# Optimization experiments

Measured on AMD Instinct MI355X. Metric: run time of the kernel, lower is better.

Reference implementation:

```python
import jax, jax.numpy as jnp
import numpy as np

U, V, A = 100000, 50000, 5000   # n_users, n_videos, n_vloggers
D = 64                           # latent_dim_rec
N_LAYERS = 3                     # VAGNN_n_layers
NNZ_UI, NNZ_UA, NNZ_G2, NNZ_G4 = 4_000_000, 2_000_000, 200_000, 2_000_000
BATCH = 1024

def spmm(rows, cols, vals, x, n_rows):
    # sparse.mm(COO(rows, cols, vals), x) -> [n_rows, d]
    return jax.ops.segment_sum(vals[:, None] * x[cols], rows, num_segments=n_rows)

def one_propagate(rows, cols, vals, a_feat, b_feat):
    # LightGCN propagation: mean over layer-0..n embeddings (running sum, no stack)
    n = a_feat.shape[0] + b_feat.shape[0]
    feats = jnp.concatenate([a_feat, b_feat], axis=0)
    acc, cur = feats, feats
    for _ in range(N_LAYERS):
        cur = spmm(rows, cols, vals, cur, n)
        acc = acc + cur
    light = acc / (N_LAYERS + 1)
    return light[:a_feat.shape[0]], light[a_feat.shape[0]:]

def l2norm(x):
    # F.normalize(x, dim=1), eps=1e-12
    return x / jnp.maximum(jnp.linalg.norm(x, axis=1, keepdims=True), 1e-12)

def setup_inputs() -> dict:
    key = jax.random.key(0)
    ks = jax.random.split(key, 16)
    return {
        'emb_user':    jax.random.normal(ks[0], (U, D), jnp.float32) * 0.1,
        'emb_video':   jax.random.normal(ks[1], (V, D), jnp.float32) * 0.1,
        'emb_vlogger': jax.random.normal(ks[2], (A, D), jnp.float32) * 0.1,
        'q':           jax.random.normal(ks[3], (D, D), jnp.float32) * 0.1,
        'ui_rows': jax.random.randint(ks[4], (NNZ_UI,), 0, U + V, jnp.int32),
        'ui_cols': jax.random.randint(ks[5], (NNZ_UI,), 0, U + V, jnp.int32),
        'ui_vals': jax.random.uniform(ks[6], (NNZ_UI,), jnp.float32) * 0.01,
        'ua_rows': jax.random.randint(ks[7], (NNZ_UA,), 0, U + A, jnp.int32),
        'ua_cols': jax.random.randint(ks[8], (NNZ_UA,), 0, U + A, jnp.int32),
        'ua_vals': jax.random.uniform(ks[9], (NNZ_UA,), jnp.float32) * 0.01,
        'g2_rows': jax.random.randint(ks[10], (NNZ_G2,), 0, A, jnp.int32),
        'g2_cols': jax.random.randint(ks[11], (NNZ_G2,), 0, V, jnp.int32),
        'g2_vals': jax.random.uniform(ks[12], (NNZ_G2,), jnp.float32) * 0.01,
        'g4_rows': jax.random.randint(ks[13], (NNZ_G4,), 0, V, jnp.int32),
        'g4_cols': jax.random.randint(ks[14], (NNZ_G4,), 0, U, jnp.int32),
        'g4_vals': jax.random.uniform(ks[15], (NNZ_G4,), jnp.float32) * 0.01,
        'vlogger_list': jax.random.randint(jax.random.fold_in(key, 100), (V,), 0, A, jnp.int32),
        'users': jax.random.randint(jax.random.fold_in(key, 101), (BATCH,), 0, U, jnp.int32),
    }

def reference(emb_user, emb_video, emb_vlogger, q,
              ui_rows, ui_cols, ui_vals,
              ua_rows, ua_cols, ua_vals,
              g2_rows, g2_cols, g2_vals,
              g4_rows, g4_cols, g4_vals,
              vlogger_list, users):
    # computer()
    atom_u, atom_v = one_propagate(ui_rows, ui_cols, ui_vals, emb_user, emb_video)
    atom_a = l2norm(spmm(g2_rows, g2_cols, g2_vals, atom_v, A))
    non_u, non_a = one_propagate(ua_rows, ua_cols, ua_vals, emb_user, emb_vlogger)
    non_v = l2norm(spmm(g4_rows, g4_cols, g4_vals, non_u, V))
    # getUsersRating()
    u_a, u_n = atom_u[users], non_u[users]                 # [B, D]
    vl_a, vl_n = atom_a[vlogger_list], non_a[vlogger_list]  # [V, D]
    ui = jax.nn.sigmoid(u_a @ atom_v.T + u_n @ non_v.T)      # [B, V]
    ua = jax.nn.sigmoid(u_a @ vl_a.T + u_n @ vl_n.T)         # [B, V]
    vid = (atom_v + non_v) * 0.5
    vlog = (vl_a + vl_n) * 0.5
    w = jax.nn.sigmoid(jnp.sum((vid @ q) * vlog, axis=1))    # [V]
    return w * ui + (1.0 - w) * ua
```

## Files before the change

### kernel.cpp

```cpp
#include <hip/hip_runtime.h>
#include <hip/hip_bf16.h>

#define U_N 100000
#define V_N 50000
#define A_N 5000

typedef float4 f4;
typedef unsigned int u32;
typedef __attribute__((ext_vector_type(8))) short bf16x8;
typedef __attribute__((ext_vector_type(4))) float f32x4;

__device__ inline float bflo(u32 p) { return __uint_as_float(p << 16); }
__device__ inline float bfhi(u32 p) { return __uint_as_float(p & 0xffff0000u); }
__device__ inline u32 f2bf(float f) {
  u32 u = __float_as_uint(f);
  return (u + 0x7fffu + ((u >> 16) & 1u)) >> 16;
}
__device__ inline u32 pack2(float lo, float hi) {
  return f2bf(lo) | (f2bf(hi) << 16);
}
__device__ inline bf16x8 ld8(const u32* p) {
  uint4 u = *(const uint4*)p;
  return __builtin_bit_cast(bf16x8, u);
}

__global__ void k_concat2b(const float* __restrict__ a, int na,
                           const float* __restrict__ b, int nb,
                           u32* __restrict__ curH, float* __restrict__ acc) {
  int total4 = (na + nb) * 16;
  for (int i = blockIdx.x * blockDim.x + threadIdx.x; i < total4;
       i += gridDim.x * blockDim.x) {
    int fi = i * 4;
    f4 v = (fi < na * 64) ? *(const f4*)(a + fi)
                          : *(const f4*)(b + (fi - na * 64));
    *(f4*)(acc + fi) = v;
    uint2 h; h.x = pack2(v.x, v.y); h.y = pack2(v.z, v.w);
    *(uint2*)(curH + (fi >> 1)) = h;
  }
}

__global__ void k_count(const int* __restrict__ rows, int nnz, int* __restrict__ cnt) {
  for (int i = blockIdx.x * blockDim.x + threadIdx.x; i < nnz;
       i += gridDim.x * blockDim.x)
    atomicAdd(&cnt[rows[i]], 1);
}

__global__ void k_bsum(const int* __restrict__ cnt, int n, int* __restrict__ bsum) {
  __shared__ int red[1024];
  int t = threadIdx.x;
  int i = blockIdx.x * 1024 + t;
  red[t] = (i < n) ? cnt[i] : 0;
  __syncthreads();
  for (int off = 512; off; off >>= 1) {
    if (t < off) red[t] += red[t + off];
    __syncthreads();
  }
  if (t == 0) bsum[blockIdx.x] = red[0];
}

__global__ void k_bscan(int* __restrict__ bsum, int nb) {
  if (threadIdx.x == 0) {
    int run = 0;
    for (int i = 0; i < nb; ++i) {
      int c = bsum[i];
      bsum[i] = run;
      run += c;
    }
  }
}

__global__ void k_bapply(const int* __restrict__ cnt, int n,
                         const int* __restrict__ bsum,
                         int* __restrict__ rp, int* __restrict__ pos) {
  __shared__ int sc[1024];
  int t = threadIdx.x;
  int i = blockIdx.x * 1024 + t;
  int c = (i < n) ? cnt[i] : 0;
  sc[t] = c;
  __syncthreads();
  #pragma unroll
  for (int off = 1; off < 1024; off <<= 1) {
    int v = (t >= off) ? sc[t - off] : 0;
    __syncthreads();
    sc[t] += v;
    __syncthreads();
  }
  int val = bsum[blockIdx.x] + sc[t] - c;
  if (i < n) {
    rp[i] = val;
    pos[i] = val;
    if (i == n - 1) rp[n] = val + c;
  }
}

__global__ void k_fillw(const int* __restrict__ rows, const int* __restrict__ cols,
                        const float* __restrict__ vals, int nnz,
                        int* __restrict__ pos, int2* __restrict__ ep,
                        int nrows, int win) {
  int tid = blockIdx.x * blockDim.x + threadIdx.x;
  int stride = gridDim.x * blockDim.x;
  for (int r0 = 0; r0 < nrows; r0 += win) {
    int r1 = min(r0 + win, nrows);
    for (int i = tid; i < nnz; i += stride) {
      int r = rows[i];
      if (r >= r0 && r < r1) {
        int slot = atomicAdd(&pos[r], 1);
        ep[slot] = make_int2(cols[i], __float_as_int(vals[i]));
      }
    }
  }
}

__global__ void k_mark(const int* __restrict__ users, int nb,
                       int* __restrict__ flag, int* __restrict__ rcount,
                       int* __restrict__ rlist) {
  int b = blockIdx.x * blockDim.x + threadIdx.x;
  if (b < nb) {
    int u = users[b];
    if (atomicExch(&flag[u], 1) == 0) {
      int m = atomicAdd(rcount, 1);
      rlist[m] = u;
    }
  }
}

__device__ __forceinline__ void spmm_row(
    int row, const int* __restrict__ rp, const int2* __restrict__ ep,
    const u32* __restrict__ inH, int instrU,
    u32* __restrict__ outH, int ostrU, int ocolU,
    float* __restrict__ acc, int l2n, int wout, int lane, int eg, int du) {
  int e0 = rp[row], e1 = rp[row + 1];
  float s[8] = {0.f, 0.f, 0.f, 0.f, 0.f, 0.f, 0.f, 0.f};
  int e = e0 + eg;
  for (; e + 8 < e1; e += 16) {
    int2 ed0 = ep[e];
    int2 ed1 = ep[e + 8];
    float v0 = __int_as_float(ed0.y), v1 = __int_as_float(ed1.y);
    uint4 x0 = *(const uint4*)(inH + (size_t)ed0.x * instrU + du);
    uint4 x1 = *(const uint4*)(inH + (size_t)ed1.x * instrU + du);
    s[0] = fmaf(v0, bflo(x0.x), s[0]); s[1] = fmaf(v0, bfhi(x0.x), s[1]);
    s[2] = fmaf(v0, bflo(x0.y), s[2]); s[3] = fmaf(v0, bfhi(x0.y), s[3]);
    s[4] = fmaf(v0, bflo(x0.z), s[4]); s[5] = fmaf(v0, bfhi(x0.z), s[5]);
    s[6] = fmaf(v0, bflo(x0.w), s[6]); s[7] = fmaf(v0, bfhi(x0.w), s[7]);
    s[0] = fmaf(v1, bflo(x1.x), s[0]); s[1] = fmaf(v1, bfhi(x1.x), s[1]);
    s[2] = fmaf(v1, bflo(x1.y), s[2]); s[3] = fmaf(v1, bfhi(x1.y), s[3]);
    s[4] = fmaf(v1, bflo(x1.z), s[4]); s[5] = fmaf(v1, bfhi(x1.z), s[5]);
    s[6] = fmaf(v1, bflo(x1.w), s[6]); s[7] = fmaf(v1, bfhi(x1.w), s[7]);
  }
  if (e < e1) {
    int2 ed0 = ep[e];
    float v0 = __int_as_float(ed0.y);
    uint4 x0 = *(const uint4*)(inH + (size_t)ed0.x * instrU + du);
    s[0] = fmaf(v0, bflo(x0.x), s[0]); s[1] = fmaf(v0, bfhi(x0.x), s[1]);
    s[2] = fmaf(v0, bflo(x0.y), s[2]); s[3] = fmaf(v0, bfhi(x0.y), s[3]);
    s[4] = fmaf(v0, bflo(x0.z), s[4]); s[5] = fmaf(v0, bfhi(x0.z), s[5]);
    s[6] = fmaf(v0, bflo(x0.w), s[6]); s[7] = fmaf(v0, bfhi(x0.w), s[7]);
  }
  #pragma unroll
  for (int j = 0; j < 8; ++j) {
    s[j] += __shfl_xor(s[j], 8);
    s[j] += __shfl_xor(s[j], 16);
    s[j] += __shfl_xor(s[j], 32);
  }
  if (l2n) {
    float ss = 0.f;
    #pragma unroll
    for (int j = 0; j < 8; ++j) ss = fmaf(s[j], s[j], ss);
    ss += __shfl_xor(ss, 1);
    ss += __shfl_xor(ss, 2);
    ss += __shfl_xor(ss, 4);
    float inv = 1.0f / fmaxf(sqrtf(ss), 1e-12f);
    #pragma unroll
    for (int j = 0; j < 8; ++j) s[j] *= inv;
  }
  if (eg == 0) {
    if (wout) {
      uint4 o;
      o.x = pack2(s[0], s[1]); o.y = pack2(s[2], s[3]);
      o.z = pack2(s[4], s[5]); o.w = pack2(s[6], s[7]);
      *(uint4*)(outH + (size_t)row * ostrU + ocolU + du) = o;
    }
    if (acc) {
      float* ap = acc + (size_t)row * 64 + (lane & 7) * 8;
      f4 a0 = *(f4*)ap, a1 = *(f4*)(ap + 4);
      a0.x += s[0]; a0.y += s[1]; a0.z += s[2]; a0.w += s[3];
      a1.x += s[4]; a1.y += s[5]; a1.z += s[6]; a1.w += s[7];
      *(f4*)ap = a0; *(f4*)(ap + 4) = a1;
    }
  }
}

__global__ void k_spmm_b(const int* __restrict__ rp, const int2* __restrict__ ep,
                         int nrows, int rbase,
                         const u32* __restrict__ inH, int instrU,
                         u32* __restrict__ outH, int ostrU, int ocolU,
                         float* __restrict__ acc, int l2n, int wout) {
  int lane = threadIdx.x & 63;
  int w = (blockIdx.x * blockDim.x + threadIdx.x) >> 6;
  int nw = (gridDim.x * blockDim.x) >> 6;
  int eg = lane >> 3;
  int du = (lane & 7) * 4;
  for (int r = w; r < nrows; r += nw)
    spmm_row(rbase + r, rp, ep, inH, instrU, outH, ostrU, ocolU, acc, l2n, wout,
             lane, eg, du);
}

__global__ void k_spmm_b_list(const int* __restrict__ rp, const int2* __restrict__ ep,
                              const int* __restrict__ rlist, const int* __restrict__ rcount,
                              const u32* __restrict__ inH, int instrU,
                              float* __restrict__ acc) {
  int lane = threadIdx.x & 63;
  int w = (blockIdx.x * blockDim.x + threadIdx.x) >> 6;
  int nw = (gridDim.x * blockDim.x) >> 6;
  int eg = lane >> 3;
  int du = (lane & 7) * 4;
  int m = *rcount;
  for (int r = w; r < m; r += nw)
    spmm_row(rlist[r], rp, ep, inH, instrU, nullptr, 0, 0, acc, 0, 0,
             lane, eg, du);
}

__global__ void k_scale_ua(float* __restrict__ acc, u32* __restrict__ UAuH) {
  int total4 = (U_N + A_N) * 16;
  for (int i = blockIdx.x * blockDim.x + threadIdx.x; i < total4;
       i += gridDim.x * blockDim.x) {
    int fi = i * 4;
    f4 v = *(f4*)(acc + fi);
    v.x *= 0.25f; v.y *= 0.25f; v.z *= 0.25f; v.w *= 0.25f;
    *(f4*)(acc + fi) = v;
    if (fi < U_N * 64) {
      uint2 h; h.x = pack2(v.x, v.y); h.y = pack2(v.z, v.w);
      *(uint2*)(UAuH + (fi >> 1)) = h;
    }
  }
}

__global__ void k_scale_ui(float* __restrict__ acc, u32* __restrict__ VAH) {
  int total4 = (U_N + V_N) * 16;
  for (int i = blockIdx.x * blockDim.x + threadIdx.x; i < total4;
       i += gridDim.x * blockDim.x) {
    int fi = i * 4;
    f4 v = *(f4*)(acc + fi);
    v.x *= 0.25f; v.y *= 0.25f; v.z *= 0.25f; v.w *= 0.25f;
    *(f4*)(acc + fi) = v;
    if (fi >= U_N * 64) {
      int rem = fi - U_N * 64;
      int row = rem >> 6, col = rem & 63;
      uint2 h; h.x = pack2(v.x, v.y); h.y = pack2(v.z, v.w);
      *(uint2*)(VAH + (size_t)row * 64 + (col >> 1)) = h;
    }
  }
}

__global__ void k_gather_u(const int* __restrict__ users,
                           const float* __restrict__ accUI,
                           const float* __restrict__ accUA,
                           u32* __restrict__ UcatH) {
  int b = blockIdx.x;
  int t = threadIdx.x;
  int u = users[b];
  UcatH[b * 64 + t] = pack2(accUI[(size_t)u * 64 + 2 * t], accUI[(size_t)u * 64 + 2 * t + 1]);
  UcatH[b * 64 + 32 + t] = pack2(accUA[(size_t)u * 64 + 2 * t], accUA[(size_t)u * 64 + 2 * t + 1]);
}

__global__ void k_gather_vb(const int* __restrict__ vlist,
                            const u32* __restrict__ atomAH,
                            const float* __restrict__ accUA,
                            u32* __restrict__ VBH) {
  int v = blockIdx.x * 4 + (threadIdx.x >> 5);
  int t = threadIdx.x & 31;
  int a = vlist[v];
  VBH[(size_t)v * 64 + t] = atomAH[(size_t)a * 32 + t];
  VBH[(size_t)v * 64 + 32 + t] =
      pack2(accUA[(size_t)(U_N + a) * 64 + 2 * t], accUA[(size_t)(U_N + a) * 64 + 2 * t + 1]);
}

__global__ void k_w(const u32* __restrict__ VAH, const u32* __restrict__ VBH,
                    const float* __restrict__ q, float* __restrict__ wv) {
  __shared__ float qs[64 * 64];
  for (int i = threadIdx.x; i < 4096; i += blockDim.x) qs[i] = q[i];
  __syncthreads();
  int lane = threadIdx.x & 63;
  int v = blockIdx.x * 4 + (threadIdx.x >> 6);
  if (v >= V_N) return;
  int half = lane & 1;
  u32 pa0 = VAH[(size_t)v * 64 + (lane >> 1)];
  u32 pa1 = VAH[(size_t)v * 64 + 32 + (lane >> 1)];
  u32 pb0 = VBH[(size_t)v * 64 + (lane >> 1)];
  u32 pb1 = VBH[(size_t)v * 64 + 32 + (lane >> 1)];
  float vid = 0.5f * ((half ? bfhi(pa0) : bflo(pa0)) + (half ? bfhi(pa1) : bflo(pa1)));
  float vlog = 0.5f * ((half ? bfhi(pb0) : bflo(pb0)) + (half ? bfhi(pb1) : bflo(pb1)));
  float s = 0.0f;
  for (int d = 0; d < 64; ++d)
    s = fmaf(__shfl(vid, d, 64), qs[d * 64 + lane], s);
  float t = s * vlog;
  #pragma unroll
  for (int off = 32; off; off >>= 1) t += __shfl_xor(t, off, 64);
  if (lane == 0) wv[v] = 1.0f / (1.0f + __expf(-t));
}

#define SPAD 68
__global__ __launch_bounds__(256) void k_rating_mfma(
    const u32* __restrict__ UcatH, const u32* __restrict__ VAH,
    const u32* __restrict__ VBH, const float* __restrict__ wv,
    float* __restrict__ out) {
  __shared__ u32 sVA[64 * SPAD];
  __shared__ u32 sVB[64 * SPAD];
  int t = threadIdx.x;
  int n0 = blockIdx.x * 64;
  for (int i = t; i < 1024; i += 256) {
    int row = i >> 4, c4 = (i & 15) * 4;
    int v = n0 + row;
    uint4 a = make_uint4(0, 0, 0, 0), b = make_uint4(0, 0, 0, 0);
    if (v < V_N) {
      a = *(const uint4*)(VAH + (size_t)v * 64 + c4);
      b = *(const uint4*)(VBH + (size_t)v * 64 + c4);
    }
    *(uint4*)(&sVA[row * SPAD + c4]) = a;
    *(uint4*)(&sVB[row * SPAD + c4]) = b;
  }
  __syncthreads();
  int lane = t & 63, wave = t >> 6;
  int m0 = (blockIdx.y * 4 + wave) * 32;
  int rr = lane & 15, g = lane >> 4;
  f32x4 accA[2][4], accB[2][4];
  #pragma unroll
  for (int i = 0; i < 2; ++i)
    #pragma unroll
    for (int j = 0; j < 4; ++j) {
      accA[i][j] = (f32x4){0.f, 0.f, 0.f, 0.f};
      accB[i][j] = (f32x4){0.f, 0.f, 0.f, 0.f};
    }
  const u32* uc0 = UcatH + (size_t)(m0 + rr) * 64 + g * 4;
  #pragma unroll
  for (int ks = 0; ks < 4; ++ks) {
    bf16x8 a0 = ld8(uc0 + ks * 16);
    bf16x8 a1 = ld8(uc0 + 16 * 64 + ks * 16);
    #pragma unroll
    for (int j = 0; j < 4; ++j) {
      int so = (j * 16 + rr) * SPAD + ks * 16 + g * 4;
      bf16x8 bA = __builtin_bit_cast(bf16x8, *(const uint4*)(&sVA[so]));
      bf16x8 bB = __builtin_bit_cast(bf16x8, *(const uint4*)(&sVB[so]));
      accA[0][j] = __builtin_amdgcn_mfma_f32_16x16x32_bf16(a0, bA, accA[0][j], 0, 0, 0);
      accA[1][j] = __builtin_amdgcn_mfma_f32_16x16x32_bf16(a1, bA, accA[1][j], 0, 0, 0);
      accB[0][j] = __builtin_amdgcn_mfma_f32_16x16x32_bf16(a0, bB, accB[0][j], 0, 0, 0);
      accB[1][j] = __builtin_amdgcn_mfma_f32_16x16x32_bf16(a1, bB, accB[1][j], 0, 0, 0);
    }
  }
  #pragma unroll
  for (int j = 0; j < 4; ++j) {
    int v = n0 + j * 16 + rr;
    if (v >= V_N) continue;
    float wvv = wv[v];
    #pragma unroll
    for (int i = 0; i < 2; ++i) {
      #pragma unroll
      for (int reg = 0; reg < 4; ++reg) {
        int u = m0 + i * 16 + g * 4 + reg;
        float sa = 1.0f / (1.0f + __expf(-accA[i][j][reg]));
        float sb = 1.0f / (1.0f + __expf(-accB[i][j][reg]));
        __builtin_nontemporal_store(wvv * sa + (1.0f - wvv) * sb,
                                    &out[(size_t)u * V_N + v]);
      }
    }
  }
}

extern "C" void kernel_launch(void* const* d_in, const int* in_sizes, int n_in,
                              void* d_out, int out_size, void* d_ws, size_t ws_size,
                              hipStream_t stream) {
  const float* emb_user    = (const float*)d_in[0];
  const float* emb_video   = (const float*)d_in[1];
  const float* emb_vlogger = (const float*)d_in[2];
  const float* q           = (const float*)d_in[3];
  const int*   ui_rows = (const int*)d_in[4];
  const int*   ui_cols = (const int*)d_in[5];
  const float* ui_vals = (const float*)d_in[6];
  const int*   ua_rows = (const int*)d_in[7];
  const int*   ua_cols = (const int*)d_in[8];
  const float* ua_vals = (const float*)d_in[9];
  const int*   g2_rows = (const int*)d_in[10];
  const int*   g2_cols = (const int*)d_in[11];
  const float* g2_vals = (const float*)d_in[12];
  const int*   g4_rows = (const int*)d_in[13];
  const int*   g4_cols = (const int*)d_in[14];
  const float* g4_vals = (const float*)d_in[15];
  const int*   vlist   = (const int*)d_in[16];
  const int*   users   = (const int*)d_in[17];
  int nnz_ui = in_sizes[4], nnz_ua = in_sizes[7];
  int nnz_g2 = in_sizes[10], nnz_g4 = in_sizes[13];

  float* ws = (float*)d_ws;
  float* accUI = ws;
  float* accUA = ws + 9600000;
  u32*   curH  = (u32*)(ws + 16320000);
  u32*   nxtH  = (u32*)(ws + 21120000);
  u32*   VAH   = (u32*)(ws + 25920000);
  u32*   VBH   = (u32*)(ws + 29120000);
  u32*   UAuH  = (u32*)(ws + 32320000);
  u32*   UcatH = (u32*)(ws + 35520000);
  u32*   atomAH= (u32*)(ws + 35585536);
  float* wv    = ws + 35745536;
  int*   bsum  = (int*)(ws + 35795536);
  int*   ib    = (int*)(ws + 35800000);
  int*   flag   = (int*)VBH;
  int*   rcount = flag + 100000;
  int*   rlist  = flag + 100016;

  const int nUI = U_N + V_N, nUA = U_N + A_N;
  auto nr_pad = [](int nrows) { return (size_t)((nrows + 1 + 15) & ~15); };

  auto build_csr = [&](const int* rows, const int* cols, const float* vals,
                       int nnz, int nrows, int win, int* rp, int* pos, int2* ep) {
    hipMemsetAsync(pos, 0, (size_t)nrows * 4, stream);
    k_count<<<2048, 256, 0, stream>>>(rows, nnz, pos);
    int nb = (nrows + 1023) / 1024;
    k_bsum<<<nb, 1024, 0, stream>>>(pos, nrows, bsum);
    k_bscan<<<1, 64, 0, stream>>>(bsum, nb);
    k_bapply<<<nb, 1024, 0, stream>>>(pos, nrows, bsum, rp, pos);
    k_fillw<<<2048, 256, 0, stream>>>(rows, cols, vals, nnz, pos, ep, nrows, win);
  };

  {
    size_t NR = nr_pad(nUI);
    int* rp = ib; int* pos = ib + NR; int2* ep = (int2*)(ib + 2 * NR);
    build_csr(ui_rows, ui_cols, ui_vals, nnz_ui, nUI, 65536, rp, pos, ep);
    k_concat2b<<<2048, 256, 0, stream>>>(emb_user, U_N, emb_video, V_N, curH, accUI);
    hipMemsetAsync(flag, 0, (size_t)(100016) * 4, stream);
    k_mark<<<4, 256, 0, stream>>>(users, 1024, flag, rcount, rlist);
    k_spmm_b<<<2048, 256, 0, stream>>>(rp, ep, nUI, 0, curH, 32, nxtH, 32, 0, accUI, 0, 1);
    k_spmm_b<<<2048, 256, 0, stream>>>(rp, ep, nUI, 0, nxtH, 32, curH, 32, 0, accUI, 0, 1);
    k_spmm_b<<<2048, 256, 0, stream>>>(rp, ep, V_N, U_N, curH, 32, nullptr, 0, 0, accUI, 0, 0);
    k_spmm_b_list<<<256, 256, 0, stream>>>(rp, ep, rlist, rcount, curH, 32, accUI);
  }
  {
    size_t NR = nr_pad(nUA);
    int* rp = ib; int* pos = ib + NR; int2* ep = (int2*)(ib + 2 * NR);
    build_csr(ua_rows, ua_cols, ua_vals, nnz_ua, nUA, 65536, rp, pos, ep);
    k_concat2b<<<2048, 256, 0, stream>>>(emb_user, U_N, emb_vlogger, A_N, curH, accUA);
    k_spmm_b<<<2048, 256, 0, stream>>>(rp, ep, nUA, 0, curH, 32, nxtH, 32, 0, accUA, 0, 1);
    k_spmm_b<<<2048, 256, 0, stream>>>(rp, ep, nUA, 0, nxtH, 32, curH, 32, 0, accUA, 0, 1);
    k_spmm_b<<<2048, 256, 0, stream>>>(rp, ep, nUA, 0, curH, 32, nullptr, 0, 0, accUA, 0, 0);
  }
  k_scale_ua<<<2048, 256, 0, stream>>>(accUA, UAuH);
  k_scale_ui<<<2048, 256, 0, stream>>>(accUI, VAH);
  size_t NR4 = nr_pad(V_N), NR2 = nr_pad(A_N);
  int* rp4 = ib; int* pos4 = ib + NR4; int2* ep4 = (int2*)(ib + 2 * NR4);
  int* ib2 = (int*)(ep4 + nnz_g4);
  int* rp2 = ib2; int* pos2 = ib2 + NR2; int2* ep2 = (int2*)(ib2 + 2 * NR2);
  build_csr(g4_rows, g4_cols, g4_vals, nnz_g4, V_N, 65536, rp4, pos4, ep4);
  build_csr(g2_rows, g2_cols, g2_vals, nnz_g2, A_N, 65536, rp2, pos2, ep2);
  k_spmm_b<<<2048, 256, 0, stream>>>(rp2, ep2, A_N, 0, VAH, 64, atomAH, 32, 0, nullptr, 1, 1);
  k_spmm_b<<<2048, 256, 0, stream>>>(rp4, ep4, V_N, 0, UAuH, 32, VAH, 64, 32, nullptr, 1, 1);
  k_gather_u<<<1024, 32, 0, stream>>>(users, accUI, accUA, UcatH);
  k_gather_vb<<<12500, 128, 0, stream>>>(vlist, atomAH, accUA, VBH);
  k_w<<<12500, 256, 0, stream>>>(VAH, VBH, q, wv);
  dim3 gridR((V_N + 63) / 64, 1024 / 128);
  k_rating_mfma<<<gridR, 256, 0, stream>>>(UcatH, VAH, VBH, wv, (float*)d_out);
}
```

Before: 1.501 ms.

## Build CSR via binned partition pass then per-bin scatter flush

Replaces the windowed fill kernel, which re-read all COO entries once per 65536-row window, with a two-phase build. A wave-level ballot partition first stages the edges into row-range bins in scratch buffers (reusing the accumulator and embedding buffers). A flush pass then scatters each bin into the CSR, so the atomics and writes stay localized. The small g2 graph uses a simple single-pass fill. This adds an extra staging write and read plus a serial loop over bins per wave, and depends on the reused scratch buffers being dead at that point.

```diff
diff --git a/kernel.cpp b/kernel.cpp
--- a/kernel.cpp
+++ b/kernel.cpp
@@ -93,20 +93,98 @@
   }
 }
 
-__global__ void k_fillw(const int* __restrict__ rows, const int* __restrict__ cols,
-                        const float* __restrict__ vals, int nnz,
-                        int* __restrict__ pos, int2* __restrict__ ep,
-                        int nrows, int win) {
+__global__ void k_fill(const int* __restrict__ rows, const int* __restrict__ cols,
+                       const float* __restrict__ vals, int nnz,
+                       int* __restrict__ pos, int2* __restrict__ ep) {
+  for (int i = blockIdx.x * blockDim.x + threadIdx.x; i < nnz;
+       i += gridDim.x * blockDim.x) {
+    int slot = atomicAdd(&pos[rows[i]], 1);
+    ep[slot] = make_int2(cols[i], __float_as_int(vals[i]));
+  }
+}
+
+__global__ void k_seedb(const int* __restrict__ rp, int binsh, int nbins,
+                        int* __restrict__ bcur) {
+  int b = threadIdx.x;
+  if (b < nbins) bcur[b] = rp[b << binsh];
+}
+
+__global__ void k_part(const int* __restrict__ rows, const int* __restrict__ cols,
+                       const float* __restrict__ vals, int nnz,
+                       int binsh, int nbins, int* __restrict__ bcur,
+                       int4* __restrict__ stg) {
+  int lane = threadIdx.x & 63;
+  int wid = (blockIdx.x * blockDim.x + threadIdx.x) >> 6;
+  int nw = (gridDim.x * blockDim.x) >> 6;
+  int nbatch = (nnz + 1023) >> 10;
+  unsigned long long lmask = (lane == 63) ? 0x7fffffffffffffffull
+                                          : ((1ull << lane) - 1ull);
+  for (int q = wid; q < nbatch; q += nw) {
+    int base = q << 10;
+    int rA[16], cA[16], bA[16];
+    float vA[16];
+    bool full = (base + 1024 <= nnz);
+    #pragma unroll
+    for (int j = 0; j < 4; ++j) {
+      int idx = base + j * 256 + lane * 4;
+      if (full) {
+        int4 r4 = *(const int4*)(rows + idx);
+        int4 c4 = *(const int4*)(cols + idx);
+        f4  v4 = *(const f4*)(vals + idx);
+        rA[j*4+0]=r4.x; rA[j*4+1]=r4.y; rA[j*4+2]=r4.z; rA[j*4+3]=r4.w;
+        cA[j*4+0]=c4.x; cA[j*4+1]=c4.y; cA[j*4+2]=c4.z; cA[j*4+3]=c4.w;
+        vA[j*4+0]=v4.x; vA[j*4+1]=v4.y; vA[j*4+2]=v4.z; vA[j*4+3]=v4.w;
+      } else {
+        #pragma unroll
+        for (int k = 0; k < 4; ++k) {
+          int e = idx + k;
+          if (e < nnz) { rA[j*4+k]=rows[e]; cA[j*4+k]=cols[e]; vA[j*4+k]=vals[e]; }
+          else { rA[j*4+k] = -1; cA[j*4+k] = 0; vA[j*4+k] = 0.f; }
+        }
+      }
+    }
+    #pragma unroll
+    for (int jj = 0; jj < 16; ++jj)
+      bA[jj] = (rA[jj] >= 0) ? (rA[jj] >> binsh) : -1;
+    for (int b = 0; b < nbins; ++b) {
+      unsigned long long m[16];
+      int n[16], tot = 0;
+      #pragma unroll
+      for (int jj = 0; jj < 16; ++jj) {
+        m[jj] = __ballot(bA[jj] == b);
+        n[jj] = __popcll(m[jj]);
+        tot += n[jj];
+      }
+      if (tot == 0) continue;
+      int g = 0;
+      if (lane == 0) g = atomicAdd(&bcur[b], tot);
+      g = __shfl(g, 0, 64);
+      int run = 0;
+      #pragma unroll
+      for (int jj = 0; jj < 16; ++jj) {
+        if (bA[jj] == b) {
+          int off = g + run + __popcll(m[jj] & lmask);
+          stg[off] = make_int4(rA[jj], cA[jj], __float_as_int(vA[jj]), 0);
+        }
+        run += n[jj];
+      }
+    }
+  }
+}
+
+__global__ void k_flush(const int4* __restrict__ stg, const int* __restrict__ rp,
+                        int nrows, int binsh, int nbins,
+                        int* __restrict__ pos, int2* __restrict__ ep) {
   int tid = blockIdx.x * blockDim.x + threadIdx.x;
   int stride = gridDim.x * blockDim.x;
-  for (int r0 = 0; r0 < nrows; r0 += win) {
-    int r1 = min(r0 + win, nrows);
-    for (int i = tid; i < nnz; i += stride) {
-      int r = rows[i];
-      if (r >= r0 && r < r1) {
-        int slot = atomicAdd(&pos[r], 1);
-        ep[slot] = make_int2(cols[i], __float_as_int(vals[i]));
-      }
+  for (int b = 0; b < nbins; ++b) {
+    int s = rp[b << binsh];
+    int r1 = min((b + 1) << binsh, nrows);
+    int e = rp[r1];
+    for (int idx = s + tid; idx < e; idx += stride) {
+      int4 ed = stg[idx];
+      int slot = atomicAdd(&pos[ed.x], 1);
+      ep[slot] = make_int2(ed.y, ed.z);
     }
   }
 }
@@ -402,7 +480,10 @@
   u32*   atomAH= (u32*)(ws + 35585536);
   float* wv    = ws + 35745536;
   int*   bsum  = (int*)(ws + 35795536);
+  int*   bcur  = (int*)(ws + 35795808);
   int*   ib    = (int*)(ws + 35800000);
+  int4*  stgUI = (int4*)accUI;
+  int4*  stgCN = (int4*)curH;
   int*   flag   = (int*)VBH;
   int*   rcount = flag + 100000;
   int*   rlist  = flag + 100016;
@@ -410,21 +491,35 @@
   const int nUI = U_N + V_N, nUA = U_N + A_N;
   auto nr_pad = [](int nrows) { return (size_t)((nrows + 1 + 15) & ~15); };
 
-  auto build_csr = [&](const int* rows, const int* cols, const float* vals,
-                       int nnz, int nrows, int win, int* rp, int* pos, int2* ep) {
+  auto build_rp = [&](const int* rows, int nnz, int nrows, int* rp, int* pos) {
     hipMemsetAsync(pos, 0, (size_t)nrows * 4, stream);
     k_count<<<2048, 256, 0, stream>>>(rows, nnz, pos);
     int nb = (nrows + 1023) / 1024;
     k_bsum<<<nb, 1024, 0, stream>>>(pos, nrows, bsum);
     k_bscan<<<1, 64, 0, stream>>>(bsum, nb);
     k_bapply<<<nb, 1024, 0, stream>>>(pos, nrows, bsum, rp, pos);
-    k_fillw<<<2048, 256, 0, stream>>>(rows, cols, vals, nnz, pos, ep, nrows, win);
+  };
+
+  auto build_csr_part = [&](const int* rows, const int* cols, const float* vals,
+                            int nnz, int nrows, int binsh, int* rp, int* pos,
+                            int2* ep, int4* stg) {
+    build_rp(rows, nnz, nrows, rp, pos);
+    int nbins = (nrows + (1 << binsh) - 1) >> binsh;
+    k_seedb<<<1, 64, 0, stream>>>(rp, binsh, nbins, bcur);
+    k_part<<<1024, 256, 0, stream>>>(rows, cols, vals, nnz, binsh, nbins, bcur, stg);
+    k_flush<<<2048, 256, 0, stream>>>(stg, rp, nrows, binsh, nbins, pos, ep);
+  };
+
+  auto build_csr_simple = [&](const int* rows, const int* cols, const float* vals,
+                              int nnz, int nrows, int* rp, int* pos, int2* ep) {
+    build_rp(rows, nnz, nrows, rp, pos);
+    k_fill<<<2048, 256, 0, stream>>>(rows, cols, vals, nnz, pos, ep);
   };
 
   {
     size_t NR = nr_pad(nUI);
     int* rp = ib; int* pos = ib + NR; int2* ep = (int2*)(ib + 2 * NR);
-    build_csr(ui_rows, ui_cols, ui_vals, nnz_ui, nUI, 65536, rp, pos, ep);
+    build_csr_part(ui_rows, ui_cols, ui_vals, nnz_ui, nUI, 14, rp, pos, ep, stgUI);
     k_concat2b<<<2048, 256, 0, stream>>>(emb_user, U_N, emb_video, V_N, curH, accUI);
     hipMemsetAsync(flag, 0, (size_t)(100016) * 4, stream);
     k_mark<<<4, 256, 0, stream>>>(users, 1024, flag, rcount, rlist);
@@ -436,7 +531,7 @@
   {
     size_t NR = nr_pad(nUA);
     int* rp = ib; int* pos = ib + NR; int2* ep = (int2*)(ib + 2 * NR);
-    build_csr(ua_rows, ua_cols, ua_vals, nnz_ua, nUA, 65536, rp, pos, ep);
+    build_csr_part(ua_rows, ua_cols, ua_vals, nnz_ua, nUA, 14, rp, pos, ep, stgCN);
     k_concat2b<<<2048, 256, 0, stream>>>(emb_user, U_N, emb_vlogger, A_N, curH, accUA);
     k_spmm_b<<<2048, 256, 0, stream>>>(rp, ep, nUA, 0, curH, 32, nxtH, 32, 0, accUA, 0, 1);
     k_spmm_b<<<2048, 256, 0, stream>>>(rp, ep, nUA, 0, nxtH, 32, curH, 32, 0, accUA, 0, 1);
@@ -448,8 +543,8 @@
   int* rp4 = ib; int* pos4 = ib + NR4; int2* ep4 = (int2*)(ib + 2 * NR4);
   int* ib2 = (int*)(ep4 + nnz_g4);
   int* rp2 = ib2; int* pos2 = ib2 + NR2; int2* ep2 = (int2*)(ib2 + 2 * NR2);
-  build_csr(g4_rows, g4_cols, g4_vals, nnz_g4, V_N, 65536, rp4, pos4, ep4);
-  build_csr(g2_rows, g2_cols, g2_vals, nnz_g2, A_N, 65536, rp2, pos2, ep2);
+  build_csr_part(g4_rows, g4_cols, g4_vals, nnz_g4, V_N, 13, rp4, pos4, ep4, stgCN);
+  build_csr_simple(g2_rows, g2_cols, g2_vals, nnz_g2, A_N, rp2, pos2, ep2);
   k_spmm_b<<<2048, 256, 0, stream>>>(rp2, ep2, A_N, 0, VAH, 64, atomAH, 32, 0, nullptr, 1, 1);
   k_spmm_b<<<2048, 256, 0, stream>>>(rp4, ep4, V_N, 0, UAuH, 32, VAH, 64, 32, nullptr, 1, 1);
   k_gather_u<<<1024, 32, 0, stream>>>(users, accUI, accUA, UcatH);
```

Result: slower. 2.284 ms (+52.2%).

## Batch CSR construction for all four graphs and merge independent kernels

Applied to the files above, without the earlier changes.

The four COO-to-CSR builds are merged into shared multi-segment kernels (zero, count, block-sum, scan, apply, fill), so each stage runs once for all graphs instead of once per graph. This cuts launch count and lets small, independent jobs fill the GPU together. The two scale kernels and the two final SpMMs are merged into split-grid launches, and the count loop now reads row indices as int4. Fill window sizes change, and the workspace is re-laid out so all CSRs can live at once by reusing other buffers (VBH, curH, atomAH), which risks aliasing bugs.

```diff
diff --git a/kernel.cpp b/kernel.cpp
--- a/kernel.cpp
+++ b/kernel.cpp
@@ -39,42 +39,92 @@
   }
 }
 
-__global__ void k_count(const int* __restrict__ rows, int nnz, int* __restrict__ cnt) {
-  for (int i = blockIdx.x * blockDim.x + threadIdx.x; i < nnz;
-       i += gridDim.x * blockDim.x)
+__global__ void k_zero4(int* p0, int n0, int* p1, int n1,
+                        int* p2, int n2, int* p3, int n3) {
+  int tid = blockIdx.x * blockDim.x + threadIdx.x;
+  int stride = gridDim.x * blockDim.x;
+  for (int i = tid; i < n0; i += stride) p0[i] = 0;
+  for (int i = tid; i < n1; i += stride) p1[i] = 0;
+  for (int i = tid; i < n2; i += stride) p2[i] = 0;
+  for (int i = tid; i < n3; i += stride) p3[i] = 0;
+}
+
+__global__ void k_count4(const int* __restrict__ r0, int n0, int* __restrict__ c0,
+                         const int* __restrict__ r1, int n1, int* __restrict__ c1,
+                         const int* __restrict__ r2, int n2, int* __restrict__ c2,
+                         const int* __restrict__ r3, int n3, int* __restrict__ c3,
+                         int s1, int s2, int s3) {
+  const int* rows; int nnz; int* cnt; int base, nb;
+  int b = blockIdx.x;
+  if (b < s1)      { rows = r0; nnz = n0; cnt = c0; base = 0;  nb = s1; }
+  else if (b < s2) { rows = r1; nnz = n1; cnt = c1; base = s1; nb = s2 - s1; }
+  else if (b < s3) { rows = r2; nnz = n2; cnt = c2; base = s2; nb = s3 - s2; }
+  else             { rows = r3; nnz = n3; cnt = c3; base = s3; nb = gridDim.x - s3; }
+  int tid = (b - base) * blockDim.x + threadIdx.x;
+  int stride = nb * blockDim.x;
+  int nq = nnz >> 2;
+  for (int q = tid; q < nq; q += stride) {
+    int4 r4 = *(const int4*)(rows + q * 4);
+    atomicAdd(&cnt[r4.x], 1);
+    atomicAdd(&cnt[r4.y], 1);
+    atomicAdd(&cnt[r4.z], 1);
+    atomicAdd(&cnt[r4.w], 1);
+  }
+  for (int i = nq * 4 + tid; i < nnz; i += stride)
     atomicAdd(&cnt[rows[i]], 1);
 }
 
-__global__ void k_bsum(const int* __restrict__ cnt, int n, int* __restrict__ bsum) {
+__global__ void k_bsum4(const int* __restrict__ c0, int n0,
+                        const int* __restrict__ c1, int n1,
+                        const int* __restrict__ c2, int n2,
+                        const int* __restrict__ c3, int n3,
+                        int b1, int b2, int b3, int* __restrict__ bsum) {
   __shared__ int red[1024];
+  const int* cnt; int n; int lb;
+  int b = blockIdx.x;
+  if (b < b1)      { cnt = c0; n = n0; lb = b; }
+  else if (b < b2) { cnt = c1; n = n1; lb = b - b1; }
+  else if (b < b3) { cnt = c2; n = n2; lb = b - b2; }
+  else             { cnt = c3; n = n3; lb = b - b3; }
   int t = threadIdx.x;
-  int i = blockIdx.x * 1024 + t;
+  int i = lb * 1024 + t;
   red[t] = (i < n) ? cnt[i] : 0;
   __syncthreads();
   for (int off = 512; off; off >>= 1) {
     if (t < off) red[t] += red[t + off];
     __syncthreads();
   }
-  if (t == 0) bsum[blockIdx.x] = red[0];
-}
-
-__global__ void k_bscan(int* __restrict__ bsum, int nb) {
+  if (t == 0) bsum[b] = red[0];
+}
+
+__global__ void k_bscan4(int* __restrict__ bsum, int b1, int b2, int b3, int btot) {
   if (threadIdx.x == 0) {
-    int run = 0;
-    for (int i = 0; i < nb; ++i) {
-      int c = bsum[i];
-      bsum[i] = run;
-      run += c;
-    }
-  }
-}
-
-__global__ void k_bapply(const int* __restrict__ cnt, int n,
-                         const int* __restrict__ bsum,
-                         int* __restrict__ rp, int* __restrict__ pos) {
+    int starts[5] = {0, b1, b2, b3, btot};
+    for (int g = 0; g < 4; ++g) {
+      int run = 0;
+      for (int i = starts[g]; i < starts[g + 1]; ++i) {
+        int c = bsum[i];
+        bsum[i] = run;
+        run += c;
+      }
+    }
+  }
+}
+
+__global__ void k_bapply4(const int* __restrict__ c0, int n0, int* __restrict__ rp0, int* __restrict__ ps0,
+                          const int* __restrict__ c1, int n1, int* __restrict__ rp1, int* __restrict__ ps1,
+                          const int* __restrict__ c2, int n2, int* __restrict__ rp2, int* __restrict__ ps2,
+                          const int* __restrict__ c3, int n3, int* __restrict__ rp3, int* __restrict__ ps3,
+                          int b1, int b2, int b3, const int* __restrict__ bsum) {
   __shared__ int sc[1024];
+  const int* cnt; int n; int* rp; int* pos; int lb;
+  int b = blockIdx.x;
+  if (b < b1)      { cnt = c0; n = n0; rp = rp0; pos = ps0; lb = b; }
+  else if (b < b2) { cnt = c1; n = n1; rp = rp1; pos = ps1; lb = b - b1; }
+  else if (b < b3) { cnt = c2; n = n2; rp = rp2; pos = ps2; lb = b - b2; }
+  else             { cnt = c3; n = n3; rp = rp3; pos = ps3; lb = b - b3; }
   int t = threadIdx.x;
-  int i = blockIdx.x * 1024 + t;
+  int i = lb * 1024 + t;
   int c = (i < n) ? cnt[i] : 0;
   sc[t] = c;
   __syncthreads();
@@ -85,7 +135,7 @@
     sc[t] += v;
     __syncthreads();
   }
-  int val = bsum[blockIdx.x] + sc[t] - c;
+  int val = bsum[b] + sc[t] - c;
   if (i < n) {
     rp[i] = val;
     pos[i] = val;
@@ -93,12 +143,25 @@
   }
 }
 
-__global__ void k_fillw(const int* __restrict__ rows, const int* __restrict__ cols,
-                        const float* __restrict__ vals, int nnz,
-                        int* __restrict__ pos, int2* __restrict__ ep,
-                        int nrows, int win) {
-  int tid = blockIdx.x * blockDim.x + threadIdx.x;
-  int stride = gridDim.x * blockDim.x;
+__global__ void k_fill2(const int* __restrict__ rA, const int* __restrict__ cA,
+                        const float* __restrict__ vA, int nnzA,
+                        int* __restrict__ posA, int2* __restrict__ epA,
+                        int nrowsA, int winA,
+                        const int* __restrict__ rB, const int* __restrict__ cB,
+                        const float* __restrict__ vB, int nnzB,
+                        int* __restrict__ posB, int2* __restrict__ epB,
+                        int nrowsB, int winB, int split) {
+  const int* rows; const int* cols; const float* vals;
+  int nnz, nrows, win; int* pos; int2* ep; int lb, nb;
+  if (blockIdx.x < split) {
+    rows = rA; cols = cA; vals = vA; nnz = nnzA; pos = posA; ep = epA;
+    nrows = nrowsA; win = winA; lb = blockIdx.x; nb = split;
+  } else {
+    rows = rB; cols = cB; vals = vB; nnz = nnzB; pos = posB; ep = epB;
+    nrows = nrowsB; win = winB; lb = blockIdx.x - split; nb = gridDim.x - split;
+  }
+  int tid = lb * blockDim.x + threadIdx.x;
+  int stride = nb * blockDim.x;
   for (int r0 = 0; r0 < nrows; r0 += win) {
     int r1 = min(r0 + win, nrows);
     for (int i = tid; i < nnz; i += stride) {
@@ -205,6 +268,33 @@
              lane, eg, du);
 }
 
+__global__ void k_spmm2(const int* __restrict__ rpA, const int2* __restrict__ epA,
+                        int nrowsA, const u32* __restrict__ inA, int instrA,
+                        u32* __restrict__ outA, int ostrA, int ocolA,
+                        const int* __restrict__ rpB, const int2* __restrict__ epB,
+                        int nrowsB, const u32* __restrict__ inB, int instrB,
+                        u32* __restrict__ outB, int ostrB, int ocolB,
+                        int split) {
+  const int* rp; const int2* ep; int nrows; const u32* inH; int instrU;
+  u32* outH; int ostrU, ocolU; int lb, nbk;
+  if (blockIdx.x < split) {
+    rp = rpA; ep = epA; nrows = nrowsA; inH = inA; instrU = instrA;
+    outH = outA; ostrU = ostrA; ocolU = ocolA; lb = blockIdx.x; nbk = split;
+  } else {
+    rp = rpB; ep = epB; nrows = nrowsB; inH = inB; instrU = instrB;
+    outH = outB; ostrU = ostrB; ocolU = ocolB;
+    lb = blockIdx.x - split; nbk = gridDim.x - split;
+  }
+  int lane = threadIdx.x & 63;
+  int w = (lb * blockDim.x + threadIdx.x) >> 6;
+  int nw = (nbk * blockDim.x) >> 6;
+  int eg = lane >> 3;
+  int du = (lane & 7) * 4;
+  for (int r = w; r < nrows; r += nw)
+    spmm_row(r, rp, ep, inH, instrU, outH, ostrU, ocolU, nullptr, 1, 1,
+             lane, eg, du);
+}
+
 __global__ void k_spmm_b_list(const int* __restrict__ rp, const int2* __restrict__ ep,
                               const int* __restrict__ rlist, const int* __restrict__ rcount,
                               const u32* __restrict__ inH, int instrU,
@@ -220,34 +310,38 @@
              lane, eg, du);
 }
 
-__global__ void k_scale_ua(float* __restrict__ acc, u32* __restrict__ UAuH) {
-  int total4 = (U_N + A_N) * 16;
-  for (int i = blockIdx.x * blockDim.x + threadIdx.x; i < total4;
-       i += gridDim.x * blockDim.x) {
-    int fi = i * 4;
-    f4 v = *(f4*)(acc + fi);
-    v.x *= 0.25f; v.y *= 0.25f; v.z *= 0.25f; v.w *= 0.25f;
-    *(f4*)(acc + fi) = v;
-    if (fi < U_N * 64) {
-      uint2 h; h.x = pack2(v.x, v.y); h.y = pack2(v.z, v.w);
-      *(uint2*)(UAuH + (fi >> 1)) = h;
-    }
-  }
-}
-
-__global__ void k_scale_ui(float* __restrict__ acc, u32* __restrict__ VAH) {
-  int total4 = (U_N + V_N) * 16;
-  for (int i = blockIdx.x * blockDim.x + threadIdx.x; i < total4;
-       i += gridDim.x * blockDim.x) {
-    int fi = i * 4;
-    f4 v = *(f4*)(acc + fi);
-    v.x *= 0.25f; v.y *= 0.25f; v.z *= 0.25f; v.w *= 0.25f;
-    *(f4*)(acc + fi) = v;
-    if (fi >= U_N * 64) {
-      int rem = fi - U_N * 64;
-      int row = rem >> 6, col = rem & 63;
-      uint2 h; h.x = pack2(v.x, v.y); h.y = pack2(v.z, v.w);
-      *(uint2*)(VAH + (size_t)row * 64 + (col >> 1)) = h;
+__global__ void k_scale2(float* __restrict__ accUI, u32* __restrict__ VAH,
+                         float* __restrict__ accUA, u32* __restrict__ UAuH,
+                         int split) {
+  if (blockIdx.x < split) {
+    int total4 = (U_N + V_N) * 16;
+    int tid = blockIdx.x * blockDim.x + threadIdx.x;
+    int stride = split * blockDim.x;
+    for (int i = tid; i < total4; i += stride) {
+      int fi = i * 4;
+      f4 v = *(f4*)(accUI + fi);
+      v.x *= 0.25f; v.y *= 0.25f; v.z *= 0.25f; v.w *= 0.25f;
+      *(f4*)(accUI + fi) = v;
+      if (fi >= U_N * 64) {
+        int rem = fi - U_N * 64;
+        int row = rem >> 6, col = rem & 63;
+        uint2 h; h.x = pack2(v.x, v.y); h.y = pack2(v.z, v.w);
+        *(uint2*)(VAH + (size_t)row * 64 + (col >> 1)) = h;
+      }
+    }
+  } else {
+    int total4 = (U_N + A_N) * 16;
+    int tid = (blockIdx.x - split) * blockDim.x + threadIdx.x;
+    int stride = (gridDim.x - split) * blockDim.x;
+    for (int i = tid; i < total4; i += stride) {
+      int fi = i * 4;
+      f4 v = *(f4*)(accUA + fi);
+      v.x *= 0.25f; v.y *= 0.25f; v.z *= 0.25f; v.w *= 0.25f;
+      *(f4*)(accUA + fi) = v;
+      if (fi < U_N * 64) {
+        uint2 h; h.x = pack2(v.x, v.y); h.y = pack2(v.z, v.w);
+        *(uint2*)(UAuH + (fi >> 1)) = h;
+      }
     }
   }
 }
@@ -402,56 +496,66 @@
   u32*   atomAH= (u32*)(ws + 35585536);
   float* wv    = ws + 35745536;
   int*   bsum  = (int*)(ws + 35795536);
-  int*   ib    = (int*)(ws + 35800000);
-  int*   flag   = (int*)VBH;
+  int*   rpUI  = (int*)(ws + 35800000);
+  int*   posUI = rpUI + 150016;
+  int2*  epUI  = (int2*)(rpUI + 300032);
+  int*   rp4   = (int*)VBH;
+  int*   pos4  = rp4 + 50016;
+  int*   rp2   = rp4 + 100032;
+  int*   pos2  = rp4 + 105040;
+  int*   rpUA  = rp4 + 110048;
+  int*   posUA = rpUA + 105008;
+  int2*  epUA  = (int2*)(rpUA + 210016);
+  int2*  ep4   = (int2*)curH;
+  int2*  ep2   = (int2*)(ws + 20320000);
+  int*   flag   = (int*)atomAH;
   int*   rcount = flag + 100000;
   int*   rlist  = flag + 100016;
 
   const int nUI = U_N + V_N, nUA = U_N + A_N;
-  auto nr_pad = [](int nrows) { return (size_t)((nrows + 1 + 15) & ~15); };
-
-  auto build_csr = [&](const int* rows, const int* cols, const float* vals,
-                       int nnz, int nrows, int win, int* rp, int* pos, int2* ep) {
-    hipMemsetAsync(pos, 0, (size_t)nrows * 4, stream);
-    k_count<<<2048, 256, 0, stream>>>(rows, nnz, pos);
-    int nb = (nrows + 1023) / 1024;
-    k_bsum<<<nb, 1024, 0, stream>>>(pos, nrows, bsum);
-    k_bscan<<<1, 64, 0, stream>>>(bsum, nb);
-    k_bapply<<<nb, 1024, 0, stream>>>(pos, nrows, bsum, rp, pos);
-    k_fillw<<<2048, 256, 0, stream>>>(rows, cols, vals, nnz, pos, ep, nrows, win);
-  };
-
-  {
-    size_t NR = nr_pad(nUI);
-    int* rp = ib; int* pos = ib + NR; int2* ep = (int2*)(ib + 2 * NR);
-    build_csr(ui_rows, ui_cols, ui_vals, nnz_ui, nUI, 65536, rp, pos, ep);
-    k_concat2b<<<2048, 256, 0, stream>>>(emb_user, U_N, emb_video, V_N, curH, accUI);
-    hipMemsetAsync(flag, 0, (size_t)(100016) * 4, stream);
-    k_mark<<<4, 256, 0, stream>>>(users, 1024, flag, rcount, rlist);
-    k_spmm_b<<<2048, 256, 0, stream>>>(rp, ep, nUI, 0, curH, 32, nxtH, 32, 0, accUI, 0, 1);
-    k_spmm_b<<<2048, 256, 0, stream>>>(rp, ep, nUI, 0, nxtH, 32, curH, 32, 0, accUI, 0, 1);
-    k_spmm_b<<<2048, 256, 0, stream>>>(rp, ep, V_N, U_N, curH, 32, nullptr, 0, 0, accUI, 0, 0);
-    k_spmm_b_list<<<256, 256, 0, stream>>>(rp, ep, rlist, rcount, curH, 32, accUI);
-  }
-  {
-    size_t NR = nr_pad(nUA);
-    int* rp = ib; int* pos = ib + NR; int2* ep = (int2*)(ib + 2 * NR);
-    build_csr(ua_rows, ua_cols, ua_vals, nnz_ua, nUA, 65536, rp, pos, ep);
-    k_concat2b<<<2048, 256, 0, stream>>>(emb_user, U_N, emb_vlogger, A_N, curH, accUA);
-    k_spmm_b<<<2048, 256, 0, stream>>>(rp, ep, nUA, 0, curH, 32, nxtH, 32, 0, accUA, 0, 1);
-    k_spmm_b<<<2048, 256, 0, stream>>>(rp, ep, nUA, 0, nxtH, 32, curH, 32, 0, accUA, 0, 1);
-    k_spmm_b<<<2048, 256, 0, stream>>>(rp, ep, nUA, 0, curH, 32, nullptr, 0, 0, accUA, 0, 0);
-  }
-  k_scale_ua<<<2048, 256, 0, stream>>>(accUA, UAuH);
-  k_scale_ui<<<2048, 256, 0, stream>>>(accUI, VAH);
-  size_t NR4 = nr_pad(V_N), NR2 = nr_pad(A_N);
-  int* rp4 = ib; int* pos4 = ib + NR4; int2* ep4 = (int2*)(ib + 2 * NR4);
-  int* ib2 = (int*)(ep4 + nnz_g4);
-  int* rp2 = ib2; int* pos2 = ib2 + NR2; int2* ep2 = (int2*)(ib2 + 2 * NR2);
-  build_csr(g4_rows, g4_cols, g4_vals, nnz_g4, V_N, 65536, rp4, pos4, ep4);
-  build_csr(g2_rows, g2_cols, g2_vals, nnz_g2, A_N, 65536, rp2, pos2, ep2);
-  k_spmm_b<<<2048, 256, 0, stream>>>(rp2, ep2, A_N, 0, VAH, 64, atomAH, 32, 0, nullptr, 1, 1);
-  k_spmm_b<<<2048, 256, 0, stream>>>(rp4, ep4, V_N, 0, UAuH, 32, VAH, 64, 32, nullptr, 1, 1);
+
+  k_zero4<<<512, 256, 0, stream>>>(posUI, nUI, posUA, nUA, pos4, V_N, pos2, A_N);
+  k_count4<<<2048, 256, 0, stream>>>(ui_rows, nnz_ui, posUI,
+                                     ua_rows, nnz_ua, posUA,
+                                     g4_rows, nnz_g4, pos4,
+                                     g2_rows, nnz_g2, pos2,
+                                     1000, 1500, 2000);
+  int nbUI = (nUI + 1023) / 1024, nbUA = (nUA + 1023) / 1024;
+  int nb4 = (V_N + 1023) / 1024, nb2 = (A_N + 1023) / 1024;
+  int b1 = nbUI, b2 = b1 + nbUA, b3 = b2 + nb4, btot = b3 + nb2;
+  k_bsum4<<<btot, 1024, 0, stream>>>(posUI, nUI, posUA, nUA, pos4, V_N, pos2, A_N,
+                                     b1, b2, b3, bsum);
+  k_bscan4<<<1, 64, 0, stream>>>(bsum, b1, b2, b3, btot);
+  k_bapply4<<<btot, 1024, 0, stream>>>(posUI, nUI, rpUI, posUI,
+                                       posUA, nUA, rpUA, posUA,
+                                       pos4, V_N, rp4, pos4,
+                                       pos2, A_N, rp2, pos2,
+                                       b1, b2, b3, bsum);
+  k_fill2<<<2048, 256, 0, stream>>>(ui_rows, ui_cols, ui_vals, nnz_ui, posUI, epUI,
+                                    nUI, 16384,
+                                    ua_rows, ua_cols, ua_vals, nnz_ua, posUA, epUA,
+                                    nUA, 16384, 1536);
+  hipMemsetAsync(flag, 0, (size_t)100016 * 4, stream);
+  k_mark<<<4, 256, 0, stream>>>(users, 1024, flag, rcount, rlist);
+
+  k_concat2b<<<2048, 256, 0, stream>>>(emb_user, U_N, emb_video, V_N, curH, accUI);
+  k_spmm_b<<<2048, 256, 0, stream>>>(rpUI, epUI, nUI, 0, curH, 32, nxtH, 32, 0, accUI, 0, 1);
+  k_spmm_b<<<2048, 256, 0, stream>>>(rpUI, epUI, nUI, 0, nxtH, 32, curH, 32, 0, accUI, 0, 1);
+  k_spmm_b<<<2048, 256, 0, stream>>>(rpUI, epUI, V_N, U_N, curH, 32, nullptr, 0, 0, accUI, 0, 0);
+  k_spmm_b_list<<<256, 256, 0, stream>>>(rpUI, epUI, rlist, rcount, curH, 32, accUI);
+
+  k_concat2b<<<2048, 256, 0, stream>>>(emb_user, U_N, emb_vlogger, A_N, curH, accUA);
+  k_spmm_b<<<2048, 256, 0, stream>>>(rpUA, epUA, nUA, 0, curH, 32, nxtH, 32, 0, accUA, 0, 1);
+  k_spmm_b<<<2048, 256, 0, stream>>>(rpUA, epUA, nUA, 0, nxtH, 32, curH, 32, 0, accUA, 0, 1);
+  k_spmm_b<<<2048, 256, 0, stream>>>(rpUA, epUA, nUA, 0, curH, 32, nullptr, 0, 0, accUA, 0, 0);
+
+  k_fill2<<<2048, 256, 0, stream>>>(g4_rows, g4_cols, g4_vals, nnz_g4, pos4, ep4,
+                                    V_N, 8192,
+                                    g2_rows, g2_cols, g2_vals, nnz_g2, pos2, ep2,
+                                    A_N, 1 << 20, 1920);
+  k_scale2<<<2048, 256, 0, stream>>>(accUI, VAH, accUA, UAuH, 1200);
+  k_spmm2<<<2048, 256, 0, stream>>>(rp2, ep2, A_N, VAH, 64, atomAH, 32, 0,
+                                    rp4, ep4, V_N, UAuH, 32, VAH, 64, 32, 192);
   k_gather_u<<<1024, 32, 0, stream>>>(users, accUI, accUA, UcatH);
   k_gather_vb<<<12500, 128, 0, stream>>>(vlist, atomAH, accUA, VBH);
   k_w<<<12500, 256, 0, stream>>>(VAH, VBH, q, wv);
```

New measurement: 1.391 ms. -7.3%, faster.
